# Kernel tuning notes

Hardware: AMD Instinct MI355X
Metric: run time of the kernel (lower is better)

Reference implementation:

```python
import jax, jax.numpy as jnp
import numpy as np

D_H = 128
N_RBF = 16
N_LAYERS = 3  # max(1, cfg.n_layers // 2) with n_layers=6
R_MAX = float(np.sqrt(2.0))


def _glorot(key, shape):
    fan_in, fan_out = shape[-2], shape[-1]
    lim = float(np.sqrt(6.0 / (fan_in + fan_out)))
    return jax.random.uniform(key, shape, jnp.float32, -lim, lim)


def setup_inputs() -> dict:
    key = jax.random.key(0)
    ks = iter(jax.random.split(key, 32))
    N, E, P, L = 10000, 320000, 100000, N_LAYERS
    d = D_H
    inp = {
        "xyr01": jax.random.uniform(next(ks), (N, 3), jnp.float32),
        "msg_edge_index": jax.random.randint(next(ks), (2, E), 0, N, jnp.int64),
        "cand_pairs_uv": jax.random.randint(next(ks), (P, 2), 0, N, jnp.int64),
        # node_in mlp: [3, d, d]
        "node_w1": _glorot(next(ks), (3, d)), "node_b1": jnp.zeros((d,), jnp.float32),
        "node_w2": _glorot(next(ks), (d, d)), "node_b2": jnp.zeros((d,), jnp.float32),
        # per-layer phi_m: [2d+n_rbf, d, d] (stacked over L layers)
        "pm_w1": _glorot(next(ks), (L, 2 * d + N_RBF, d)), "pm_b1": jnp.zeros((L, d), jnp.float32),
        "pm_w2": _glorot(next(ks), (L, d, d)), "pm_b2": jnp.zeros((L, d), jnp.float32),
        # per-layer phi_h: [2d, d, d]
        "ph_w1": _glorot(next(ks), (L, 2 * d, d)), "ph_b1": jnp.zeros((L, d), jnp.float32),
        "ph_w2": _glorot(next(ks), (L, d, d)), "ph_b2": jnp.zeros((L, d), jnp.float32),
        # per-layer LayerNorm
        "ln_g": jnp.ones((L, d), jnp.float32), "ln_b": jnp.zeros((L, d), jnp.float32),
        # edge_head mlp: [2d+4, d, 1]
        "eh_w1": _glorot(next(ks), (2 * d + 4, d)), "eh_b1": jnp.zeros((d,), jnp.float32),
        "eh_w2": _glorot(next(ks), (d, 1)), "eh_b2": jnp.zeros((1,), jnp.float32),
    }
    return inp


def _mlp2(x, w1, b1, w2, b2):
    # Linear -> SiLU -> Linear (dropout=0.0)
    return jax.nn.silu(x @ w1 + b1) @ w2 + b2


def _rbf(r):
    # Gaussian RBF: centers linspace(0, sqrt(2), n_rbf), width = spacing
    centers = jnp.linspace(0.0, R_MAX, N_RBF)
    width = R_MAX / (N_RBF - 1)
    gamma = 0.5 / (width * width)
    return jnp.exp(-gamma * (r[:, None] - centers) ** 2)


def _layernorm(x, g, b, eps=1e-5):
    mu = jnp.mean(x, axis=-1, keepdims=True)
    var = jnp.mean((x - mu) ** 2, axis=-1, keepdims=True)
    return (x - mu) * jax.lax.rsqrt(var + eps) * g + b


def reference(xyr01, msg_edge_index, cand_pairs_uv,
              node_w1, node_b1, node_w2, node_b2,
              pm_w1, pm_b1, pm_w2, pm_b2,
              ph_w1, ph_b1, ph_w2, ph_b2,
              ln_g, ln_b,
              eh_w1, eh_b1, eh_w2, eh_b2):
    N = xyr01.shape[0]
    src, dst = msg_edge_index[0], msg_edge_index[1]
    edge_weight = jnp.ones((msg_edge_index.shape[1],), jnp.float32)

    h = _mlp2(xyr01, node_w1, node_b1, node_w2, node_b2)  # [N, d]

    # geometric features are layer-invariant
    dx = xyr01[src, :2] - xyr01[dst, :2]
    r = jnp.sqrt(jnp.sum(dx * dx, axis=-1) + 1e-8)
    rbf = _rbf(r)  # [E, n_rbf]

    for l in range(N_LAYERS):
        m_in = jnp.concatenate([h[src], h[dst], rbf], axis=-1)  # [E, 2d+n_rbf]
        m = _mlp2(m_in, pm_w1[l], pm_b1[l], pm_w2[l], pm_b2[l])
        m = m * edge_weight[:, None]
        agg = jax.ops.segment_sum(m, dst, num_segments=N)  # [N, d]
        h_up = _mlp2(jnp.concatenate([h, agg], axis=-1), ph_w1[l], ph_b1[l], ph_w2[l], ph_b2[l])
        h = _layernorm(h + h_up, ln_g[l], ln_b[l])

    u, v = cand_pairs_uv[:, 0], cand_pairs_uv[:, 1]
    duv = xyr01[u, :2] - xyr01[v, :2]
    dist = jnp.sqrt(jnp.sum(duv * duv, axis=-1, keepdims=True) + 1e-8)
    r_pair = jnp.concatenate([xyr01[u, 2:3], xyr01[v, 2:3], dist,
                              jnp.abs(xyr01[u, 2:3] - xyr01[v, 2:3])], axis=-1)  # [P, 4]
    feat = jnp.concatenate([h[u], h[v], r_pair], axis=-1)  # [P, 2d+4]
    logits = _mlp2(feat, eh_w1, eh_b1, eh_w2, eh_b2).squeeze(-1)  # [P]
    return logits
```

## Files before the change

### kernel.cpp

```cpp
#include <hip/hip_runtime.h>

#define DH 128
#define RMAXF 1.41421356237309515f
#define TGRID 512

typedef float  floatx4 __attribute__((ext_vector_type(4)));
typedef float  floatx2 __attribute__((ext_vector_type(2)));
typedef short  shortx8 __attribute__((ext_vector_type(8)));
typedef int    intx4  __attribute__((ext_vector_type(4)));

__device__ __forceinline__ unsigned short f2bf(float f) {
    unsigned u = __builtin_bit_cast(unsigned, f);
    u += 0x7fffu + ((u >> 16) & 1u);
    return (unsigned short)(u >> 16);
}
__device__ __forceinline__ floatx2 unpack_bf2(unsigned u) {
    floatx2 r;
    r.x = __builtin_bit_cast(float, u << 16);
    r.y = __builtin_bit_cast(float, u & 0xffff0000u);
    return r;
}
__device__ __forceinline__ float fast_silu(float x) {
    return x * __builtin_amdgcn_rcpf(1.f + __expf(-x));
}

__global__ void prep_w2p_kernel(const float* __restrict__ pm_w2, const float* __restrict__ pm_b2,
                                const float* __restrict__ ph_w1,
                                float* __restrict__ W2P, float* __restrict__ cvec) {
    int idx = blockIdx.x * 256 + threadIdx.x;
    const int tot = 3 * 128 * 128;
    if (idx < tot) {
        int l = idx / (128 * 128);
        int rem = idx - l * 128 * 128;
        int k = rem >> 7, o = rem & 127;
        const float* w2r = pm_w2 + (size_t)l * 128 * 128 + (size_t)k * 128;
        const float* p1b = ph_w1 + (size_t)l * 256 * 128 + (size_t)128 * 128 + o;
        float s = 0.f;
        for (int m = 0; m < 128; ++m) s += w2r[m] * p1b[(size_t)m * 128];
        W2P[idx] = s;
        return;
    }
    idx -= tot;
    if (idx < 3 * 128) {
        int l = idx >> 7, o = idx & 127;
        const float* b2 = pm_b2 + l * 128;
        const float* p1b = ph_w1 + (size_t)l * 256 * 128 + (size_t)128 * 128 + o;
        float s = 0.f;
        for (int m = 0; m < 128; ++m) s += b2[m] * p1b[(size_t)m * 128];
        cvec[idx] = s;
    }
}

__global__ void prep_all_kernel(const float* __restrict__ pm_w1, const float* __restrict__ eh_w1,
                                const float* __restrict__ ph_w1, const float* __restrict__ ph_w2,
                                const float* __restrict__ W2P,
                                unsigned short* __restrict__ W1abT, unsigned short* __restrict__ EHT,
                                unsigned short* __restrict__ PB1T, unsigned short* __restrict__ PH2T,
                                float* __restrict__ T,
                                int* __restrict__ cnt, int N) {
    int idx = blockIdx.x * 256 + threadIdx.x;
    const int nA = 3 * 256 * 128;
    const int nB = 256 * 128;
    const int nC = 3 * 128 * 256;
    const int nD = 3 * 128 * 128;
    const int nT = 3 * (TGRID + 1) * 128;
    if (idx < nA) {
        int l = idx / (256 * 128);
        int rem = idx - l * 256 * 128;
        int j = rem >> 7, k = rem & 127;
        int srow = ((j >> 7) << 7) + k;
        W1abT[idx] = f2bf(pm_w1[(size_t)l * 272 * 128 + (size_t)srow * 128 + (j & 127)]);
        return;
    }
    idx -= nA;
    if (idx < nB) {
        int j = idx >> 7, k = idx & 127;
        int srow = ((j >> 7) << 7) + k;
        EHT[idx] = f2bf(eh_w1[(size_t)srow * 128 + (j & 127)]);
        return;
    }
    idx -= nB;
    if (idx < nC) {
        int l = idx / (128 * 256);
        int rem = idx - l * 128 * 256;
        int j = rem >> 8, k = rem & 255;
        float v = (k < 128) ? ph_w1[(size_t)l * 256 * 128 + (size_t)k * 128 + j]
                            : W2P[(size_t)l * 128 * 128 + (size_t)(k - 128) * 128 + j];
        PB1T[idx] = f2bf(v);
        return;
    }
    idx -= nC;
    if (idx < nD) {
        int l = idx / (128 * 128);
        int rem = idx - l * 128 * 128;
        int j = rem >> 7, k = rem & 127;
        PH2T[idx] = f2bf(ph_w2[(size_t)l * 128 * 128 + (size_t)k * 128 + j]);
        return;
    }
    idx -= nD;
    if (idx < nT) {
        int l = idx / ((TGRID + 1) * 128);
        int rem = idx - l * (TGRID + 1) * 128;
        int i = rem >> 7, ch = rem & 127;
        float r = (float)i * (RMAXF / (float)TGRID);
        const float step = RMAXF / 15.f;
        const float gamma = 56.25f;
        const float* w1c = pm_w1 + (size_t)l * 272 * 128 + (size_t)256 * 128 + ch;
        float s = 0.f;
#pragma unroll
        for (int k = 0; k < 16; ++k) {
            float d = r - (float)k * step;
            s += expf(-gamma * d * d) * w1c[(size_t)k * 128];
        }
        T[idx] = s;
        return;
    }
    idx -= nT;
    if (idx < N) cnt[idx] = 0;
}

__global__ __launch_bounds__(128)
void node_enc_kernel(const float* __restrict__ xyr,
                     const float* __restrict__ w1, const float* __restrict__ b1,
                     const float* __restrict__ w2, const float* __restrict__ b2,
                     float* __restrict__ h, unsigned short* __restrict__ hbf, int N) {
    __shared__ float xs[16][3];
    __shared__ float hid[16][DH];
    int n0 = blockIdx.x * 16;
    int t = threadIdx.x;
    if (t < 48) {
        int i = t / 3, j = t - 3 * (t / 3);
        int n = n0 + i; if (n >= N) n = N - 1;
        xs[i][j] = xyr[3 * n + j];
    }
    __syncthreads();
    int col = t;
    float w10 = w1[col], w11 = w1[DH + col], w12 = w1[2 * DH + col];
    float bb = b1[col];
#pragma unroll
    for (int i = 0; i < 16; ++i) {
        float v = bb + xs[i][0] * w10 + xs[i][1] * w11 + xs[i][2] * w12;
        hid[i][col] = fast_silu(v);
    }
    __syncthreads();
    float a[16];
#pragma unroll
    for (int i = 0; i < 16; ++i) a[i] = b2[col];
    for (int j = 0; j < DH; ++j) {
        float wv = w2[j * DH + col];
#pragma unroll
        for (int i = 0; i < 16; ++i) a[i] += hid[i][j] * wv;
    }
    for (int i = 0; i < 16; ++i) {
        int n = n0 + i;
        if (n < N) {
            h[(size_t)n * DH + col] = a[i];
            hbf[(size_t)n * DH + col] = f2bf(a[i]);
        }
    }
}

__global__ void count_kernel(const int* __restrict__ dst, int* __restrict__ cnt, int E) {
    int e = blockIdx.x * 256 + threadIdx.x;
    if (e < E) atomicAdd(&cnt[dst[e]], 1);
}
__global__ __launch_bounds__(1024)
void scan_kernel(const int* __restrict__ cnt, int* __restrict__ rs, int* __restrict__ cursor,
                 float* __restrict__ cntf, int N) {
    __shared__ int ps[1024];
    const int CH = 16;
    int t = threadIdx.x;
    int base = t * CH;
    int loc[CH];
    int s = 0;
#pragma unroll
    for (int j = 0; j < CH; ++j) {
        int i = base + j;
        int v = (i < N) ? cnt[i] : 0;
        if (i < N) cntf[i] = (float)v;
        loc[j] = s; s += v;
    }
    ps[t] = s;
    __syncthreads();
    for (int off = 1; off < 1024; off <<= 1) {
        int v = (t >= off) ? ps[t - off] : 0;
        __syncthreads();
        ps[t] += v;
        __syncthreads();
    }
    int pre = (t > 0) ? ps[t - 1] : 0;
#pragma unroll
    for (int j = 0; j < CH; ++j) {
        int i = base + j;
        if (i < N) { int v = pre + loc[j]; rs[i] = v; cursor[i] = v; }
    }
    if (t == 0) rs[N] = ps[1023];
}
__global__ void fill_kernel(const int* __restrict__ src, const int* __restrict__ dst,
                            int* __restrict__ cursor, const float* __restrict__ xyr,
                            int* __restrict__ esrc, float* __restrict__ rv, int E) {
    int e = blockIdx.x * 256 + threadIdx.x;
    if (e < 16) { esrc[E + e] = 0; rv[E + e] = 0.f; }
    if (e >= E) return;
    int s = src[e], d = dst[e];
    int p = atomicAdd(&cursor[d], 1);
    esrc[p] = s;
    float dx = xyr[3 * s] - xyr[3 * d];
    float dy = xyr[3 * s + 1] - xyr[3 * d + 1];
    rv[p] = sqrtf(dx * dx + dy * dy + 1e-8f);
}

__global__ __launch_bounds__(256)
void proj_kernel(const unsigned short* __restrict__ Abf,
                 const unsigned short* __restrict__ BT,
                 unsigned short* __restrict__ O1b, unsigned short* __restrict__ O2b, int M) {
    const int tid = threadIdx.x;
    const int w = tid >> 6, lane = tid & 63;
    const int mr = lane & 15, q = lane >> 4;
    const int row0 = blockIdx.x * 64;
    floatx4 acc[4][4] = {};
#pragma unroll
    for (int kc = 0; kc < 4; ++kc) {
        const int ko = kc * 32 + q * 8;
        shortx8 a[4], b[4];
#pragma unroll
        for (int mt = 0; mt < 4; ++mt) {
            int r = row0 + mt * 16 + mr; if (r >= M) r = M - 1;
            a[mt] = *reinterpret_cast<const shortx8*>(Abf + (size_t)r * DH + ko);
        }
#pragma unroll
        for (int nt = 0; nt < 4; ++nt) {
            int ocol = w * 64 + nt * 16 + mr;
            b[nt] = *reinterpret_cast<const shortx8*>(BT + (size_t)ocol * DH + ko);
        }
#pragma unroll
        for (int mt = 0; mt < 4; ++mt)
#pragma unroll
            for (int nt = 0; nt < 4; ++nt)
                acc[mt][nt] = __builtin_amdgcn_mfma_f32_16x16x32_bf16(a[mt], b[nt], acc[mt][nt], 0, 0, 0);
    }
#pragma unroll
    for (int nt = 0; nt < 4; ++nt) {
        int ocol = w * 64 + nt * 16 + mr;
        unsigned short* O = (ocol < DH) ? O1b : O2b;
        int col = ocol & (DH - 1);
#pragma unroll
        for (int mt = 0; mt < 4; ++mt)
#pragma unroll
            for (int r4 = 0; r4 < 4; ++r4) {
                int gr = row0 + mt * 16 + q * 4 + r4;
                if (gr < M) O[(size_t)gr * DH + col] = f2bf(acc[mt][nt][r4]);
            }
    }
}

__global__ __launch_bounds__(64)
void edge_kernel(const unsigned short* __restrict__ Hsb, const unsigned short* __restrict__ Hdb,
                 const float* __restrict__ T,
                 const float* __restrict__ b1,
                 const int* __restrict__ rs, const int* __restrict__ esrc,
                 const float* __restrict__ rv,
                 unsigned int* __restrict__ Sbf, int N) {
    const int n = blockIdx.x;
    const int lane = threadIdx.x;
    const int c = lane * 2;
    floatx2 hdn = unpack_bf2(*(const unsigned*)(Hdb + (size_t)n * DH + c))
                + *(const floatx2*)(b1 + c);
    const int s = rs[n], e = rs[n + 1];
    floatx2 acc = {0.f, 0.f};
    const int cnt = e - s;
    if (cnt > 0) {
        const float scale = (float)TGRID / RMAXF;
        const int nb = (cnt + 3) >> 2;
        intx4  sn = __builtin_nontemporal_load((const intx4*)(esrc + s));
        floatx4 rq = __builtin_nontemporal_load((const floatx4*)(rv + s));
        unsigned hu[4];
        hu[0] = *(const unsigned*)(Hsb + (size_t)sn.x * DH + c);
        hu[1] = *(const unsigned*)(Hsb + (size_t)sn.y * DH + c);
        hu[2] = *(const unsigned*)(Hsb + (size_t)sn.z * DH + c);
        hu[3] = *(const unsigned*)(Hsb + (size_t)sn.w * DH + c);
        for (int b = 0; b < nb; ++b) {
            const int j = s + b * 4;
            intx4  snN = __builtin_nontemporal_load((const intx4*)(esrc + j + 4));
            floatx4 rqN = __builtin_nontemporal_load((const floatx4*)(rv + j + 4));
            unsigned huN[4];
            huN[0] = *(const unsigned*)(Hsb + (size_t)snN.x * DH + c);
            huN[1] = *(const unsigned*)(Hsb + (size_t)snN.y * DH + c);
            huN[2] = *(const unsigned*)(Hsb + (size_t)snN.z * DH + c);
            huN[3] = *(const unsigned*)(Hsb + (size_t)snN.w * DH + c);
            float rr[4] = {rq.x, rq.y, rq.z, rq.w};
#pragma unroll
            for (int i = 0; i < 4; ++i) {
                float rs_ = rr[i] * scale;
                int i0 = (int)rs_;
                i0 = (i0 > TGRID - 1) ? (TGRID - 1) : i0;
                float t = rs_ - (float)i0;
                floatx2 t0 = *(const floatx2*)(T + (size_t)i0 * DH + c);
                floatx2 t1 = *(const floatx2*)(T + (size_t)(i0 + 1) * DH + c);
                floatx2 R = t0 + t * (t1 - t0);
                floatx2 pre = unpack_bf2(hu[i]) + hdn + R;
                floatx2 sg;
                sg.x = __builtin_amdgcn_rcpf(1.f + __expf(-pre.x));
                sg.y = __builtin_amdgcn_rcpf(1.f + __expf(-pre.y));
                float msk = (j + i < e) ? 1.f : 0.f;
                acc += (pre * sg) * msk;
            }
#pragma unroll
            for (int i = 0; i < 4; ++i) hu[i] = huN[i];
            sn = snN; rq = rqN;
        }
    }
    unsigned lo = f2bf(acc.x), hi = f2bf(acc.y);
    Sbf[(size_t)n * 64 + lane] = lo | (hi << 16);
}

template<int LAST>
__global__ __launch_bounds__(256)
void upd_kernel(unsigned short* hbf,
                const unsigned short* __restrict__ Sbf16,
                float* h,
                const unsigned short* __restrict__ PB1T,
                const float* __restrict__ b1v,
                const float* __restrict__ cvec,
                const float* __restrict__ cntf,
                const unsigned short* __restrict__ P2T,
                const float* __restrict__ b2v,
                const float* __restrict__ g, const float* __restrict__ bb,
                const unsigned short* __restrict__ BT,
                unsigned short* __restrict__ O1b, unsigned short* __restrict__ O2b,
                float* __restrict__ O1f, float* __restrict__ O2f,
                int M) {
    __shared__ unsigned short HID[64 * 136];
    __shared__ float red[4][64][2];
    __shared__ float stats[64][2];
    __shared__ float cntL[64];
    const int tid = threadIdx.x;
    const int w = tid >> 6, lane = tid & 63;
    const int mr = lane & 15, q = lane >> 4;
    const int row0 = blockIdx.x * 64;

    if (tid < 64) {
        int r = row0 + tid;
        cntL[tid] = (r < M) ? cntf[r] : 0.f;
    }
    __syncthreads();

    floatx4 acc[4][2] = {};
#pragma unroll
    for (int kc = 0; kc < 8; ++kc) {
        const int ko = kc * 32 + q * 8;
        shortx8 a[4], bfr[2];
#pragma unroll
        for (int mt = 0; mt < 4; ++mt) {
            int r = row0 + mt * 16 + mr; if (r >= M) r = M - 1;
            const unsigned short* sp = (ko < DH) ? (hbf + (size_t)r * DH + ko)
                                                 : (Sbf16 + (size_t)r * DH + (ko - DH));
            a[mt] = *reinterpret_cast<const shortx8*>(sp);
        }
#pragma unroll
        for (int nt = 0; nt < 2; ++nt)
            bfr[nt] = *reinterpret_cast<const shortx8*>(PB1T + (size_t)(w * 32 + nt * 16 + mr) * 256 + ko);
#pragma unroll
        for (int mt = 0; mt < 4; ++mt)
#pragma unroll
            for (int nt = 0; nt < 2; ++nt)
                acc[mt][nt] = __builtin_amdgcn_mfma_f32_16x16x32_bf16(a[mt], bfr[nt], acc[mt][nt], 0, 0, 0);
    }
#pragma unroll
    for (int nt = 0; nt < 2; ++nt) {
        int col = w * 32 + nt * 16 + mr;
        float bv = b1v[col], cv = cvec[col];
#pragma unroll
        for (int mt = 0; mt < 4; ++mt)
#pragma unroll
            for (int r4 = 0; r4 < 4; ++r4) {
                int row = mt * 16 + q * 4 + r4;
                HID[row * 136 + col] = f2bf(fast_silu(acc[mt][nt][r4] + bv + cntL[row] * cv));
            }
    }
    __syncthreads();

    floatx4 acc3[4][2] = {};
#pragma unroll
    for (int kc = 0; kc < 4; ++kc) {
        const int ko = kc * 32 + q * 8;
        shortx8 a[4], bfr[2];
#pragma unroll
        for (int mt = 0; mt < 4; ++mt)
            a[mt] = *reinterpret_cast<const shortx8*>(HID + (mt * 16 + mr) * 136 + ko);
#pragma unroll
        for (int nt = 0; nt < 2; ++nt)
            bfr[nt] = *reinterpret_cast<const shortx8*>(P2T + (size_t)(w * 32 + nt * 16 + mr) * DH + ko);
#pragma unroll
        for (int mt = 0; mt < 4; ++mt)
#pragma unroll
            for (int nt = 0; nt < 2; ++nt)
                acc3[mt][nt] = __builtin_amdgcn_mfma_f32_16x16x32_bf16(a[mt], bfr[nt], acc3[mt][nt], 0, 0, 0);
    }
#pragma unroll
    for (int nt = 0; nt < 2; ++nt) {
        int col = w * 32 + nt * 16 + mr;
        float b2c = b2v[col];
#pragma unroll
        for (int mt = 0; mt < 4; ++mt)
#pragma unroll
            for (int r4 = 0; r4 < 4; ++r4) {
                int gr = row0 + mt * 16 + q * 4 + r4;
                float hv = (gr < M) ? h[(size_t)gr * DH + col] : 0.f;
                acc3[mt][nt][r4] = acc3[mt][nt][r4] + b2c + hv;
            }
    }
#pragma unroll
    for (int mt = 0; mt < 4; ++mt)
#pragma unroll
        for (int r4 = 0; r4 < 4; ++r4) {
            float y0 = acc3[mt][0][r4], y1 = acc3[mt][1][r4];
            float s1 = y0 + y1, s2 = y0 * y0 + y1 * y1;
#pragma unroll
            for (int m = 1; m < 16; m <<= 1) {
                s1 += __shfl_xor(s1, m);
                s2 += __shfl_xor(s2, m);
            }
            if (mr == 0) {
                int row = mt * 16 + q * 4 + r4;
                red[w][row][0] = s1; red[w][row][1] = s2;
            }
        }
    __syncthreads();
    if (tid < 64) {
        float s1 = red[0][tid][0] + red[1][tid][0] + red[2][tid][0] + red[3][tid][0];
        float s2 = red[0][tid][1] + red[1][tid][1] + red[2][tid][1] + red[3][tid][1];
        float mu = s1 * (1.f / DH);
        float var = s2 * (1.f / DH) - mu * mu;
        stats[tid][0] = mu;
        stats[tid][1] = rsqrtf(var + 1e-5f);
    }
    __syncthreads();
#pragma unroll
    for (int nt = 0; nt < 2; ++nt) {
        int col = w * 32 + nt * 16 + mr;
        float gc = g[col], bc = bb[col];
#pragma unroll
        for (int mt = 0; mt < 4; ++mt)
#pragma unroll
            for (int r4 = 0; r4 < 4; ++r4) {
                int row = mt * 16 + q * 4 + r4;
                int gr = row0 + row;
                if (gr < M) {
                    float yv = (acc3[mt][nt][r4] - stats[row][0]) * stats[row][1] * gc + bc;
                    unsigned short yb = f2bf(yv);
                    h[(size_t)gr * DH + col] = yv;
                    hbf[(size_t)gr * DH + col] = yb;
                    HID[row * 136 + col] = yb;
                }
            }
    }
    __syncthreads();

    floatx4 acc4[4][4] = {};
#pragma unroll
    for (int kc = 0; kc < 4; ++kc) {
        const int ko = kc * 32 + q * 8;
        shortx8 a[4], b[4];
#pragma unroll
        for (int mt = 0; mt < 4; ++mt)
            a[mt] = *reinterpret_cast<const shortx8*>(HID + (mt * 16 + mr) * 136 + ko);
#pragma unroll
        for (int nt = 0; nt < 4; ++nt) {
            int ocol = w * 64 + nt * 16 + mr;
            b[nt] = *reinterpret_cast<const shortx8*>(BT + (size_t)ocol * DH + ko);
        }
#pragma unroll
        for (int mt = 0; mt < 4; ++mt)
#pragma unroll
            for (int nt = 0; nt < 4; ++nt)
                acc4[mt][nt] = __builtin_amdgcn_mfma_f32_16x16x32_bf16(a[mt], b[nt], acc4[mt][nt], 0, 0, 0);
    }
#pragma unroll
    for (int nt = 0; nt < 4; ++nt) {
        int ocol = w * 64 + nt * 16 + mr;
        int col = ocol & (DH - 1);
#pragma unroll
        for (int mt = 0; mt < 4; ++mt)
#pragma unroll
            for (int r4 = 0; r4 < 4; ++r4) {
                int gr = row0 + mt * 16 + q * 4 + r4;
                if (gr < M) {
                    if (LAST) {
                        float* O = (ocol < DH) ? O1f : O2f;
                        O[(size_t)gr * DH + col] = acc4[mt][nt][r4];
                    } else {
                        unsigned short* O = (ocol < DH) ? O1b : O2b;
                        O[(size_t)gr * DH + col] = f2bf(acc4[mt][nt][r4]);
                    }
                }
            }
    }
}

__global__ __launch_bounds__(256)
void pair_kernel(const float* __restrict__ Hu, const float* __restrict__ Hv,
                 const int* __restrict__ pairs, const float* __restrict__ xyr,
                 const float* __restrict__ ehw1c,
                 const float* __restrict__ eb1, const float* __restrict__ ew2,
                 const float* __restrict__ eb2,
                 float* __restrict__ out, int P) {
    int half = threadIdx.x >> 5;
    int p = blockIdx.x * 8 + half;
    bool valid = (p < P);
    int pp = valid ? p : (P - 1);
    int u = pairs[2 * pp], v = pairs[2 * pp + 1];
    float ru = xyr[3 * u + 2], rv_ = xyr[3 * v + 2];
    float dx = xyr[3 * u] - xyr[3 * v];
    float dy = xyr[3 * u + 1] - xyr[3 * v + 1];
    float dist = sqrtf(dx * dx + dy * dy + 1e-8f);
    float adr = fabsf(ru - rv_);
    int c = (threadIdx.x & 31) * 4;
    floatx4 hu = *(const floatx4*)(Hu + (size_t)u * DH + c);
    floatx4 hv = *(const floatx4*)(Hv + (size_t)v * DH + c);
    floatx4 bv = *(const floatx4*)(eb1 + c);
    floatx4 wv = *(const floatx4*)(ew2 + c);
    floatx4 c0 = *(const floatx4*)(ehw1c + 0 * DH + c);
    floatx4 c1 = *(const floatx4*)(ehw1c + 1 * DH + c);
    floatx4 c2 = *(const floatx4*)(ehw1c + 2 * DH + c);
    floatx4 c3 = *(const floatx4*)(ehw1c + 3 * DH + c);
    floatx4 px = hu + hv + bv + ru * c0 + rv_ * c1 + dist * c2 + adr * c3;
    float val = fast_silu(px.x) * wv.x + fast_silu(px.y) * wv.y +
                fast_silu(px.z) * wv.z + fast_silu(px.w) * wv.w;
#pragma unroll
    for (int m = 1; m < 32; m <<= 1) val += __shfl_xor(val, m);
    if (((threadIdx.x & 31) == 0) && valid) out[p] = val + eb2[0];
}

extern "C" void kernel_launch(void* const* d_in, const int* in_sizes, int n_in,
                              void* d_out, int out_size, void* d_ws, size_t ws_size,
                              hipStream_t stream) {
    const float* xyr     = (const float*)d_in[0];
    const int*   eidx    = (const int*)d_in[1];
    const int*   pairs   = (const int*)d_in[2];
    const float* node_w1 = (const float*)d_in[3];
    const float* node_b1 = (const float*)d_in[4];
    const float* node_w2 = (const float*)d_in[5];
    const float* node_b2 = (const float*)d_in[6];
    const float* pm_w1   = (const float*)d_in[7];
    const float* pm_b1   = (const float*)d_in[8];
    const float* pm_w2   = (const float*)d_in[9];
    const float* pm_b2   = (const float*)d_in[10];
    const float* ph_w1   = (const float*)d_in[11];
    const float* ph_b1   = (const float*)d_in[12];
    const float* ph_w2   = (const float*)d_in[13];
    const float* ph_b2   = (const float*)d_in[14];
    const float* ln_g    = (const float*)d_in[15];
    const float* ln_b    = (const float*)d_in[16];
    const float* eh_w1   = (const float*)d_in[17];
    const float* eh_b1   = (const float*)d_in[18];
    const float* eh_w2   = (const float*)d_in[19];
    const float* eh_b2   = (const float*)d_in[20];

    const int N = in_sizes[0] / 3;
    const int E = in_sizes[1] / 2;
    const int P = in_sizes[2] / 2;
    const int* src = eidx;
    const int* dst = eidx + E;

    char* ws = (char*)d_ws;
    size_t off = 0;
    auto alloc = [&](size_t bytes) -> char* {
        char* p = ws + off;
        off += (bytes + 255) & ~(size_t)255;
        return p;
    };
    unsigned short* W1abT = (unsigned short*)alloc((size_t)3 * 256 * 128 * 2);
    unsigned short* PB1T  = (unsigned short*)alloc((size_t)3 * 128 * 256 * 2);
    unsigned short* PH2T  = (unsigned short*)alloc((size_t)3 * 128 * 128 * 2);
    unsigned short* EHT   = (unsigned short*)alloc((size_t)256 * 128 * 2);
    float*          W2P   = (float*)alloc((size_t)3 * 128 * 128 * 4);
    float*          cvec  = (float*)alloc((size_t)3 * 128 * 4);
    float*          Ttab  = (float*)alloc((size_t)3 * (TGRID + 1) * 128 * 4);
    float*          h     = (float*)alloc((size_t)N * DH * 4);
    unsigned short* hbf   = (unsigned short*)alloc((size_t)N * DH * 2);
    unsigned short* Hsb   = (unsigned short*)alloc((size_t)N * DH * 2);
    unsigned short* Hdb   = (unsigned short*)alloc((size_t)N * DH * 2);
    float*          Hs    = (float*)alloc((size_t)N * DH * 4);
    float*          Hd    = (float*)alloc((size_t)N * DH * 4);
    unsigned int*   Sbf   = (unsigned int*)alloc((size_t)N * 64 * 4);
    float*          rv    = (float*)alloc((size_t)(E + 16) * 4);
    int*            esrc  = (int*)alloc((size_t)(E + 16) * 4);
    int*            cnt   = (int*)alloc((size_t)N * 4);
    int*            rs    = (int*)alloc((size_t)(N + 1) * 4);
    int*            cursor= (int*)alloc((size_t)N * 4);
    float*          cntf  = (float*)alloc((size_t)N * 4);
    (void)ws_size; (void)n_in; (void)out_size;

    const int W2P_TOT = 3 * 128 * 128 + 3 * 128;
    prep_w2p_kernel<<<(W2P_TOT + 255) / 256, 256, 0, stream>>>(pm_w2, pm_b2, ph_w1, W2P, cvec);
    const int PREP_TOT = 3 * 256 * 128 + 256 * 128 + 3 * 128 * 256 + 3 * 128 * 128
                       + 3 * (TGRID + 1) * 128 + N;
    prep_all_kernel<<<(PREP_TOT + 255) / 256, 256, 0, stream>>>(pm_w1, eh_w1, ph_w1, ph_w2, W2P,
                                                                W1abT, EHT, PB1T, PH2T, Ttab, cnt, N);

    node_enc_kernel<<<(N + 15) / 16, 128, 0, stream>>>(xyr, node_w1, node_b1, node_w2, node_b2, h, hbf, N);
    count_kernel<<<(E + 255) / 256, 256, 0, stream>>>(dst, cnt, E);
    scan_kernel<<<1, 1024, 0, stream>>>(cnt, rs, cursor, cntf, N);
    fill_kernel<<<(E + 255) / 256, 256, 0, stream>>>(src, dst, cursor, xyr, esrc, rv, E);

    const int MB = (N + 63) / 64;
    proj_kernel<<<MB, 256, 0, stream>>>(hbf, W1abT, Hsb, Hdb, N);
    for (int l = 0; l < 3; ++l) {
        edge_kernel<<<N, 64, 0, stream>>>(Hsb, Hdb, Ttab + (size_t)l * (TGRID + 1) * 128,
                                          pm_b1 + l * DH, rs, esrc, rv, Sbf, N);
        if (l < 2) {
            upd_kernel<0><<<MB, 256, 0, stream>>>(hbf, (const unsigned short*)Sbf, h,
                                                  PB1T + (size_t)l * 128 * 256, ph_b1 + l * DH,
                                                  cvec + l * 128, cntf,
                                                  PH2T + (size_t)l * 128 * 128, ph_b2 + l * DH,
                                                  ln_g + l * DH, ln_b + l * DH,
                                                  W1abT + (size_t)(l + 1) * 256 * 128,
                                                  Hsb, Hdb, nullptr, nullptr, N);
        } else {
            upd_kernel<1><<<MB, 256, 0, stream>>>(hbf, (const unsigned short*)Sbf, h,
                                                  PB1T + (size_t)l * 128 * 256, ph_b1 + l * DH,
                                                  cvec + l * 128, cntf,
                                                  PH2T + (size_t)l * 128 * 128, ph_b2 + l * DH,
                                                  ln_g + l * DH, ln_b + l * DH,
                                                  EHT, nullptr, nullptr, Hs, Hd, N);
        }
    }

    pair_kernel<<<(P + 7) / 8, 256, 0, stream>>>(Hs, Hd, pairs, xyr, eh_w1 + 256 * DH,
                                                 eh_b1, eh_w2, eh_b2, (float*)d_out, P);
}
```

Before: 368.3 us.

## Pack edge source and quantized RBF index, use bf16 nearest-neighbor table

Edges now store the source node and a quantized distance-table index packed into one int, instead of separate source and float-distance arrays. The RBF-projection table grows to a finer grid and is stored as bf16, and the edge kernel looks up the nearest entry rather than interpolating between two fp32 rows. The separate W2P precompute kernel is folded into the main prep kernel, which drops one launch but makes some prep threads run a 128-step dot product. This cuts per-edge index and table traffic and arithmetic, in exchange for nearest-neighbor quantization error and bf16 rounding in the RBF term.

```diff
diff --git a/kernel.cpp b/kernel.cpp
--- a/kernel.cpp
+++ b/kernel.cpp
@@ -2,7 +2,7 @@
 
 #define DH 128
 #define RMAXF 1.41421356237309515f
-#define TGRID 512
+#define TGRID 2048
 
 typedef float  floatx4 __attribute__((ext_vector_type(4)));
 typedef float  floatx2 __attribute__((ext_vector_type(2)));
@@ -24,45 +24,19 @@
     return x * __builtin_amdgcn_rcpf(1.f + __expf(-x));
 }
 
-__global__ void prep_w2p_kernel(const float* __restrict__ pm_w2, const float* __restrict__ pm_b2,
-                                const float* __restrict__ ph_w1,
-                                float* __restrict__ W2P, float* __restrict__ cvec) {
-    int idx = blockIdx.x * 256 + threadIdx.x;
-    const int tot = 3 * 128 * 128;
-    if (idx < tot) {
-        int l = idx / (128 * 128);
-        int rem = idx - l * 128 * 128;
-        int k = rem >> 7, o = rem & 127;
-        const float* w2r = pm_w2 + (size_t)l * 128 * 128 + (size_t)k * 128;
-        const float* p1b = ph_w1 + (size_t)l * 256 * 128 + (size_t)128 * 128 + o;
-        float s = 0.f;
-        for (int m = 0; m < 128; ++m) s += w2r[m] * p1b[(size_t)m * 128];
-        W2P[idx] = s;
-        return;
-    }
-    idx -= tot;
-    if (idx < 3 * 128) {
-        int l = idx >> 7, o = idx & 127;
-        const float* b2 = pm_b2 + l * 128;
-        const float* p1b = ph_w1 + (size_t)l * 256 * 128 + (size_t)128 * 128 + o;
-        float s = 0.f;
-        for (int m = 0; m < 128; ++m) s += b2[m] * p1b[(size_t)m * 128];
-        cvec[idx] = s;
-    }
-}
-
 __global__ void prep_all_kernel(const float* __restrict__ pm_w1, const float* __restrict__ eh_w1,
                                 const float* __restrict__ ph_w1, const float* __restrict__ ph_w2,
-                                const float* __restrict__ W2P,
+                                const float* __restrict__ pm_w2, const float* __restrict__ pm_b2,
                                 unsigned short* __restrict__ W1abT, unsigned short* __restrict__ EHT,
                                 unsigned short* __restrict__ PB1T, unsigned short* __restrict__ PH2T,
-                                float* __restrict__ T,
+                                float* __restrict__ cvec, unsigned short* __restrict__ Tb,
                                 int* __restrict__ cnt, int N) {
     int idx = blockIdx.x * 256 + threadIdx.x;
     const int nA = 3 * 256 * 128;
     const int nB = 256 * 128;
     const int nC = 3 * 128 * 256;
     const int nD = 3 * 128 * 128;
+    const int nE = 3 * 128;
     const int nT = 3 * (TGRID + 1) * 128;
     if (idx < nA) {
         int l = idx / (256 * 128);
@@ -84,8 +58,16 @@
         int l = idx / (128 * 256);
         int rem = idx - l * 128 * 256;
         int j = rem >> 8, k = rem & 255;
-        float v = (k < 128) ? ph_w1[(size_t)l * 256 * 128 + (size_t)k * 128 + j]
-                            : W2P[(size_t)l * 128 * 128 + (size_t)(k - 128) * 128 + j];
+        float v;
+        if (k < 128) {
+            v = ph_w1[(size_t)l * 256 * 128 + (size_t)k * 128 + j];
+        } else {
+            const float* w2r = pm_w2 + (size_t)l * 128 * 128 + (size_t)(k - 128) * 128;
+            const float* p1b = ph_w1 + (size_t)l * 256 * 128 + (size_t)128 * 128 + j;
+            float s = 0.f;
+            for (int m = 0; m < 128; ++m) s += w2r[m] * p1b[(size_t)m * 128];
+            v = s;
+        }
         PB1T[idx] = f2bf(v);
         return;
     }
@@ -98,6 +80,16 @@
         return;
     }
     idx -= nD;
+    if (idx < nE) {
+        int l = idx >> 7, o = idx & 127;
+        const float* b2 = pm_b2 + l * 128;
+        const float* p1b = ph_w1 + (size_t)l * 256 * 128 + (size_t)128 * 128 + o;
+        float s = 0.f;
+        for (int m = 0; m < 128; ++m) s += b2[m] * p1b[(size_t)m * 128];
+        cvec[idx] = s;
+        return;
+    }
+    idx -= nE;
     if (idx < nT) {
         int l = idx / ((TGRID + 1) * 128);
         int rem = idx - l * (TGRID + 1) * 128;
@@ -112,7 +104,7 @@
             float d = r - (float)k * step;
             s += expf(-gamma * d * d) * w1c[(size_t)k * 128];
         }
-        T[idx] = s;
+        Tb[idx] = f2bf(s);
         return;
     }
     idx -= nT;
@@ -198,16 +190,18 @@
 }
 __global__ void fill_kernel(const int* __restrict__ src, const int* __restrict__ dst,
                             int* __restrict__ cursor, const float* __restrict__ xyr,
-                            int* __restrict__ esrc, float* __restrict__ rv, int E) {
+                            int* __restrict__ epack, int E) {
     int e = blockIdx.x * 256 + threadIdx.x;
-    if (e < 16) { esrc[E + e] = 0; rv[E + e] = 0.f; }
+    if (e < 16) epack[E + e] = 0;
     if (e >= E) return;
     int s = src[e], d = dst[e];
     int p = atomicAdd(&cursor[d], 1);
-    esrc[p] = s;
     float dx = xyr[3 * s] - xyr[3 * d];
     float dy = xyr[3 * s + 1] - xyr[3 * d + 1];
-    rv[p] = sqrtf(dx * dx + dy * dy + 1e-8f);
+    float r = sqrtf(dx * dx + dy * dy + 1e-8f);
+    int ti = (int)(r * ((float)TGRID / RMAXF) + 0.5f);
+    ti = (ti > TGRID) ? TGRID : ti;
+    epack[p] = s | (ti << 18);
 }
 
 __global__ __launch_bounds__(256)
@@ -256,10 +250,9 @@
 
 __global__ __launch_bounds__(64)
 void edge_kernel(const unsigned short* __restrict__ Hsb, const unsigned short* __restrict__ Hdb,
-                 const float* __restrict__ T,
+                 const unsigned short* __restrict__ Tb,
                  const float* __restrict__ b1,
-                 const int* __restrict__ rs, const int* __restrict__ esrc,
-                 const float* __restrict__ rv,
+                 const int* __restrict__ rs, const int* __restrict__ epack,
                  unsigned int* __restrict__ Sbf, int N) {
     const int n = blockIdx.x;
     const int lane = threadIdx.x;
@@ -270,35 +263,38 @@
     floatx2 acc = {0.f, 0.f};
     const int cnt = e - s;
     if (cnt > 0) {
-        const float scale = (float)TGRID / RMAXF;
         const int nb = (cnt + 3) >> 2;
-        intx4  sn = __builtin_nontemporal_load((const intx4*)(esrc + s));
-        floatx4 rq = __builtin_nontemporal_load((const floatx4*)(rv + s));
-        unsigned hu[4];
-        hu[0] = *(const unsigned*)(Hsb + (size_t)sn.x * DH + c);
-        hu[1] = *(const unsigned*)(Hsb + (size_t)sn.y * DH + c);
-        hu[2] = *(const unsigned*)(Hsb + (size_t)sn.z * DH + c);
-        hu[3] = *(const unsigned*)(Hsb + (size_t)sn.w * DH + c);
+        intx4 pk = __builtin_nontemporal_load((const intx4*)(epack + s));
+        unsigned hu[4], tw[4];
+        {
+            int p0 = pk.x, p1 = pk.y, p2 = pk.z, p3 = pk.w;
+            hu[0] = *(const unsigned*)(Hsb + (size_t)(p0 & 0x3ffff) * DH + c);
+            hu[1] = *(const unsigned*)(Hsb + (size_t)(p1 & 0x3ffff) * DH + c);
+            hu[2] = *(const unsigned*)(Hsb + (size_t)(p2 & 0x3ffff) * DH + c);
+            hu[3] = *(const unsigned*)(Hsb + (size_t)(p3 & 0x3ffff) * DH + c);
+            tw[0] = *(const unsigned*)(Tb + (size_t)(((unsigned)p0) >> 18) * DH + c);
+            tw[1] = *(const unsigned*)(Tb + (size_t)(((unsigned)p1) >> 18) * DH + c);
+            tw[2] = *(const unsigned*)(Tb + (size_t)(((unsigned)p2) >> 18) * DH + c);
+            tw[3] = *(const unsigned*)(Tb + (size_t)(((unsigned)p3) >> 18) * DH + c);
+        }
         for (int b = 0; b < nb; ++b) {
             const int j = s + b * 4;
-            intx4  snN = __builtin_nontemporal_load((const intx4*)(esrc + j + 4));
-            floatx4 rqN = __builtin_nontemporal_load((const floatx4*)(rv + j + 4));
-            unsigned huN[4];
-            huN[0] = *(const unsigned*)(Hsb + (size_t)snN.x * DH + c);
-            huN[1] = *(const unsigned*)(Hsb + (size_t)snN.y * DH + c);
-            huN[2] = *(const unsigned*)(Hsb + (size_t)snN.z * DH + c);
-            huN[3] = *(const unsigned*)(Hsb + (size_t)snN.w * DH + c);
-            float rr[4] = {rq.x, rq.y, rq.z, rq.w};
+            intx4 pkN = __builtin_nontemporal_load((const intx4*)(epack + j + 4));
+            unsigned huN[4], twN[4];
+            {
+                int p0 = pkN.x, p1 = pkN.y, p2 = pkN.z, p3 = pkN.w;
+                huN[0] = *(const unsigned*)(Hsb + (size_t)(p0 & 0x3ffff) * DH + c);
+                huN[1] = *(const unsigned*)(Hsb + (size_t)(p1 & 0x3ffff) * DH + c);
+                huN[2] = *(const unsigned*)(Hsb + (size_t)(p2 & 0x3ffff) * DH + c);
+                huN[3] = *(const unsigned*)(Hsb + (size_t)(p3 & 0x3ffff) * DH + c);
+                twN[0] = *(const unsigned*)(Tb + (size_t)(((unsigned)p0) >> 18) * DH + c);
+                twN[1] = *(const unsigned*)(Tb + (size_t)(((unsigned)p1) >> 18) * DH + c);
+                twN[2] = *(const unsigned*)(Tb + (size_t)(((unsigned)p2) >> 18) * DH + c);
+                twN[3] = *(const unsigned*)(Tb + (size_t)(((unsigned)p3) >> 18) * DH + c);
+            }
 #pragma unroll
             for (int i = 0; i < 4; ++i) {
-                float rs_ = rr[i] * scale;
-                int i0 = (int)rs_;
-                i0 = (i0 > TGRID - 1) ? (TGRID - 1) : i0;
-                float t = rs_ - (float)i0;
-                floatx2 t0 = *(const floatx2*)(T + (size_t)i0 * DH + c);
-                floatx2 t1 = *(const floatx2*)(T + (size_t)(i0 + 1) * DH + c);
-                floatx2 R = t0 + t * (t1 - t0);
-                floatx2 pre = unpack_bf2(hu[i]) + hdn + R;
+                floatx2 pre = unpack_bf2(hu[i]) + hdn + unpack_bf2(tw[i]);
                 floatx2 sg;
                 sg.x = __builtin_amdgcn_rcpf(1.f + __expf(-pre.x));
                 sg.y = __builtin_amdgcn_rcpf(1.f + __expf(-pre.y));
@@ -306,8 +302,7 @@
                 acc += (pre * sg) * msk;
             }
 #pragma unroll
-            for (int i = 0; i < 4; ++i) hu[i] = huN[i];
-            sn = snN; rq = rqN;
+            for (int i = 0; i < 4; ++i) { hu[i] = huN[i]; tw[i] = twN[i]; }
         }
     }
     unsigned lo = f2bf(acc.x), hi = f2bf(acc.y);
@@ -574,9 +569,8 @@
     unsigned short* PB1T  = (unsigned short*)alloc((size_t)3 * 128 * 256 * 2);
     unsigned short* PH2T  = (unsigned short*)alloc((size_t)3 * 128 * 128 * 2);
     unsigned short* EHT   = (unsigned short*)alloc((size_t)256 * 128 * 2);
-    float*          W2P   = (float*)alloc((size_t)3 * 128 * 128 * 4);
     float*          cvec  = (float*)alloc((size_t)3 * 128 * 4);
-    float*          Ttab  = (float*)alloc((size_t)3 * (TGRID + 1) * 128 * 4);
+    unsigned short* Ttab  = (unsigned short*)alloc((size_t)3 * (TGRID + 1) * 128 * 2);
     float*          h     = (float*)alloc((size_t)N * DH * 4);
     unsigned short* hbf   = (unsigned short*)alloc((size_t)N * DH * 2);
     unsigned short* Hsb   = (unsigned short*)alloc((size_t)N * DH * 2);
@@ -584,31 +578,30 @@
     float*          Hs    = (float*)alloc((size_t)N * DH * 4);
     float*          Hd    = (float*)alloc((size_t)N * DH * 4);
     unsigned int*   Sbf   = (unsigned int*)alloc((size_t)N * 64 * 4);
-    float*          rv    = (float*)alloc((size_t)(E + 16) * 4);
-    int*            esrc  = (int*)alloc((size_t)(E + 16) * 4);
+    int*            epack = (int*)alloc((size_t)(E + 16) * 4);
     int*            cnt   = (int*)alloc((size_t)N * 4);
     int*            rs    = (int*)alloc((size_t)(N + 1) * 4);
     int*            cursor= (int*)alloc((size_t)N * 4);
     float*          cntf  = (float*)alloc((size_t)N * 4);
     (void)ws_size; (void)n_in; (void)out_size;
 
-    const int W2P_TOT = 3 * 128 * 128 + 3 * 128;
-    prep_w2p_kernel<<<(W2P_TOT + 255) / 256, 256, 0, stream>>>(pm_w2, pm_b2, ph_w1, W2P, cvec);
     const int PREP_TOT = 3 * 256 * 128 + 256 * 128 + 3 * 128 * 256 + 3 * 128 * 128
-                       + 3 * (TGRID + 1) * 128 + N;
-    prep_all_kernel<<<(PREP_TOT + 255) / 256, 256, 0, stream>>>(pm_w1, eh_w1, ph_w1, ph_w2, W2P,
-                                                                W1abT, EHT, PB1T, PH2T, Ttab, cnt, N);
+                       + 3 * 128 + 3 * (TGRID + 1) * 128 + N;
+    prep_all_kernel<<<(PREP_TOT + 255) / 256, 256, 0, stream>>>(pm_w1, eh_w1, ph_w1, ph_w2,
+                                                                pm_w2, pm_b2,
+                                                                W1abT, EHT, PB1T, PH2T,
+                                                                cvec, Ttab, cnt, N);
 
     node_enc_kernel<<<(N + 15) / 16, 128, 0, stream>>>(xyr, node_w1, node_b1, node_w2, node_b2, h, hbf, N);
     count_kernel<<<(E + 255) / 256, 256, 0, stream>>>(dst, cnt, E);
     scan_kernel<<<1, 1024, 0, stream>>>(cnt, rs, cursor, cntf, N);
-    fill_kernel<<<(E + 255) / 256, 256, 0, stream>>>(src, dst, cursor, xyr, esrc, rv, E);
+    fill_kernel<<<(E + 255) / 256, 256, 0, stream>>>(src, dst, cursor, xyr, epack, E);
 
     const int MB = (N + 63) / 64;
     proj_kernel<<<MB, 256, 0, stream>>>(hbf, W1abT, Hsb, Hdb, N);
     for (int l = 0; l < 3; ++l) {
         edge_kernel<<<N, 64, 0, stream>>>(Hsb, Hdb, Ttab + (size_t)l * (TGRID + 1) * 128,
-                                          pm_b1 + l * DH, rs, esrc, rv, Sbf, N);
+                                          pm_b1 + l * DH, rs, epack, Sbf, N);
         if (l < 2) {
             upd_kernel<0><<<MB, 256, 0, stream>>>(hbf, (const unsigned short*)Sbf, h,
                                                   PB1T + (size_t)l * 128 * 256, ph_b1 + l * DH,
```

New measurement: 344.2 us. -6.6%, faster.
